# Kernel tuning notes

Measured on AMD Instinct MI355X. Metric: run time of the kernel, lower is better.

The kernel has to match this reference:

```python
import jax, jax.numpy as jnp
from jax import lax
import numpy as np

B, N, D_MODEL = 4, 2048, 768
D_INNER = 1536      # int(2.0 * d_model)
DT_RANK = 48        # ceil(768 / 16)
EPS = 1e-5


def setup_inputs() -> dict:
    key = jax.random.key(0)
    ks = jax.random.split(key, 9)
    x = jax.random.normal(ks[0], (B, N, D_MODEL), jnp.float32)
    # BFS order: a permutation of node ids
    sorted_index = jax.random.permutation(ks[1], N).astype(jnp.int32)
    # parent BFS position of node at BFS position i, must be < i; root (i=0) has -1
    pos = jnp.arange(N)
    r = jax.random.randint(ks[2], (N,), 0, N)
    sorted_parent = jnp.where(pos == 0, -1, r % jnp.maximum(pos, 1)).astype(jnp.int32)
    s = 0.02
    in_proj_w = jax.random.normal(ks[3], (D_MODEL, 2 * D_INNER), jnp.float32) * s
    x_proj_w = jax.random.normal(ks[4], (D_INNER, DT_RANK + 2), jnp.float32) * s
    dt_proj_w = jax.random.normal(ks[5], (DT_RANK, D_INNER), jnp.float32) * (DT_RANK ** -0.5)
    # dt bias init: softplus^{-1}(dt) with dt ~ LogUniform(1e-3, 1e-1)
    dt = jnp.exp(jax.random.uniform(ks[6], (D_INNER,)) * (np.log(0.1) - np.log(0.001)) + np.log(0.001))
    dt_proj_b = (dt + jnp.log(-jnp.expm1(-dt))).astype(jnp.float32)
    A_log = jnp.zeros((D_INNER,), jnp.float32)   # log(A=1) per original init (d_state=1)
    D_param = jnp.ones((D_INNER,), jnp.float32)
    ln_gamma = jnp.ones((D_INNER,), jnp.float32)
    ln_beta = jnp.zeros((D_INNER,), jnp.float32)
    out_proj_w = jax.random.normal(ks[7], (D_INNER, D_MODEL), jnp.float32) * s
    return dict(x=x, sorted_index=sorted_index, sorted_parent=sorted_parent,
                in_proj_w=in_proj_w, x_proj_w=x_proj_w, dt_proj_w=dt_proj_w,
                dt_proj_b=dt_proj_b, A_log=A_log, D_param=D_param,
                ln_gamma=ln_gamma, ln_beta=ln_beta, out_proj_w=out_proj_w)


def _tree_ssm_recurrence(dBx, dA, sorted_index, sorted_parent):
    """h[bfs i] = dA[node(i)] * h[parent_bfs(i)] + dBx[node(i)]. Inputs (B,N,Di) node-major."""
    b, n, di = dBx.shape
    dA_bfs = jnp.take(dA, sorted_index, axis=1)    # (B,N,Di) in BFS order
    dBx_bfs = jnp.take(dBx, sorted_index, axis=1)

    def step(h_buf, inp):
        t, par, dA_t, dBx_t = inp                   # dA_t/dBx_t: (B,Di)
        h_par = h_buf[:, jnp.maximum(par, 0)]       # (B,Di) gather at parent BFS pos
        h_par = jnp.where(par < 0, jnp.zeros_like(h_par), h_par)
        h_t = dA_t * h_par + dBx_t
        return h_buf.at[:, t].set(h_t), h_t

    xs = (jnp.arange(n), sorted_parent,
          dA_bfs.transpose(1, 0, 2), dBx_bfs.transpose(1, 0, 2))
    _, h_bfs = lax.scan(step, jnp.zeros((b, n, di), dBx.dtype), xs)
    # scatter BFS-order states back to node-id order
    h = jnp.zeros((b, n, di), dBx.dtype).at[:, sorted_index].set(h_bfs.transpose(1, 0, 2))
    return h


def reference(x, sorted_index, sorted_parent, in_proj_w, x_proj_w, dt_proj_w,
              dt_proj_b, A_log, D_param, ln_gamma, ln_beta, out_proj_w):
    xz = x @ in_proj_w                              # (B,N,2*Di)
    x_inner, z = jnp.split(xz, 2, axis=-1)
    z = jax.nn.silu(z)
    x_dbl = x_inner @ x_proj_w                      # (B,N,dt_rank+2)
    dt_lr, B_ssm, C_ssm = (x_dbl[..., :DT_RANK], x_dbl[..., DT_RANK:DT_RANK + 1],
                           x_dbl[..., DT_RANK + 1:DT_RANK + 2])
    dt = jax.nn.softplus(dt_lr @ dt_proj_w + dt_proj_b)  # (B,N,Di)
    As = -jnp.exp(A_log)                            # (Di,) negative
    dA = jnp.exp(dt * As)                           # (B,N,Di) in (0,1)
    dBx = dt * B_ssm * x_inner                      # (B,N,Di)
    h = _tree_ssm_recurrence(dBx, dA, sorted_index, sorted_parent)
    y = h * C_ssm + D_param * x_inner               # (B,N,Di)
    mu = jnp.mean(y, axis=-1, keepdims=True)
    var = jnp.mean(jnp.square(y - mu), axis=-1, keepdims=True)
    y = (y - mu) * lax.rsqrt(var + EPS) * ln_gamma + ln_beta
    y = y * z
    return y @ out_proj_w                           # (B,N,D)
```

## Files before the change

### kernel.cpp

```cpp
#include <hip/hip_runtime.h>
#include <math.h>


#define ROWS 8192
#define DIN 1536
#define DMOD 768
#define NSEQ 2048
#define DTR 48
#define NSPLIT 8

typedef __bf16 bfrag __attribute__((ext_vector_type(8)));
typedef float f4 __attribute__((ext_vector_type(4)));

__device__ __forceinline__ unsigned short f2bf(float f) {
  unsigned int u = __float_as_uint(f);
  unsigned int r = (u + 0x7fffu + ((u >> 16) & 1u)) >> 16;
  return (unsigned short)r;
}
__device__ __forceinline__ float bf2f(unsigned short h) {
  return __uint_as_float(((unsigned int)h) << 16);
}

__device__ __forceinline__ void gld_lds16(const void* g, void* l) {
  __builtin_amdgcn_global_load_lds((const __attribute__((address_space(1))) void*)g,
                                   (__attribute__((address_space(3))) void*)l, 16, 0, 0);
}

template <int MODE>
__global__ __launch_bounds__(256) void mfma_gemm(
    const unsigned short* __restrict__ A, const unsigned short* __restrict__ Bt,
    void* __restrict__ C0v, void* __restrict__ C1v, int K, int ldc) {
  __shared__ unsigned short As[128 * 32];
  __shared__ unsigned short Bs[128 * 32];
  const int tid = threadIdx.x;
  const int w = tid >> 6, l = tid & 63;
  const int quad = l >> 4, l16 = l & 15;
  const int wrow = (w >> 1) * 64, wcol = (w & 1) * 64;
  const int row0 = blockIdx.y * 128, col0 = blockIdx.x * 128;

  f4 acc[4][4];
#pragma unroll
  for (int i = 0; i < 4; i++)
#pragma unroll
    for (int j = 0; j < 4; j++) acc[i][j] = (f4){0.f, 0.f, 0.f, 0.f};

  const int arow = row0 + w * 16 + (l >> 2);
  const int brow = col0 + w * 16 + (l >> 2);
  const int kcol = (((l & 3) ^ ((l >> 2) & 3)) * 8);
  const int qs = (quad ^ (l16 & 3)) * 8;

  for (int k0 = 0; k0 < K; k0 += 32) {
#pragma unroll
    for (int r = 0; r < 2; r++) {
      gld_lds16(A + (size_t)(arow + r * 64) * K + k0 + kcol,
                (char*)As + r * 4096 + w * 1024);
      gld_lds16(Bt + (size_t)(brow + r * 64) * K + k0 + kcol,
                (char*)Bs + r * 4096 + w * 1024);
    }
    __syncthreads();
    bfrag af[4], bf[4];
#pragma unroll
    for (int i = 0; i < 4; i++)
      af[i] = *(const bfrag*)(const void*)(As + (wrow + i * 16 + l16) * 32 + qs);
#pragma unroll
    for (int j = 0; j < 4; j++)
      bf[j] = *(const bfrag*)(const void*)(Bs + (wcol + j * 16 + l16) * 32 + qs);
#pragma unroll
    for (int i = 0; i < 4; i++)
#pragma unroll
      for (int j = 0; j < 4; j++)
        acc[i][j] = __builtin_amdgcn_mfma_f32_16x16x32_bf16(af[i], bf[j], acc[i][j], 0, 0, 0);
    __syncthreads();
  }

  if (MODE == 0) {
    float* C0 = (float*)C0v;
    const int ccol = col0 + wcol + l16;
#pragma unroll
    for (int i = 0; i < 4; i++) {
      const int rb = row0 + wrow + i * 16 + quad * 4;
#pragma unroll
      for (int j = 0; j < 4; j++)
#pragma unroll
        for (int r = 0; r < 4; r++)
          C0[(size_t)(rb + r) * ldc + ccol + j * 16] = acc[i][j][r];
    }
  } else {
    const bool is_z = (col0 >= DIN);
    unsigned short* dst = is_z ? (unsigned short*)C1v : (unsigned short*)C0v;
    const int cbase = col0 + wcol + l16 - (is_z ? DIN : 0);
#pragma unroll
    for (int i = 0; i < 4; i++) {
      const int rb = row0 + wrow + i * 16 + quad * 4;
#pragma unroll
      for (int j = 0; j < 4; j++)
#pragma unroll
        for (int r = 0; r < 4; r++) {
          float v = acc[i][j][r];
          if (is_z) v = v / (1.f + __expf(-v));
          dst[(size_t)(rb + r) * DIN + cbase + j * 16] = f2bf(v);
        }
    }
  }
}

__global__ __launch_bounds__(1024) void prep1_kernel(
    const int* __restrict__ sidx, const int* __restrict__ spar,
    int* __restrict__ SLOT_PACK, int* __restrict__ SLOTINV,
    int* __restrict__ LSTART, int* __restrict__ NLEV,
    const float* __restrict__ x, unsigned short* __restrict__ Xbf,
    const float* __restrict__ xpw, unsigned short* __restrict__ XPW,
    const float* __restrict__ dtw, unsigned short* __restrict__ DTWb,
    const float* __restrict__ A_log, float* __restrict__ negA) {
  const int bi = blockIdx.x;
  const int tid = threadIdx.x;
  if (bi == 0) {
    __shared__ int par[2048], idx[2048], ancA[2048], ancB[2048], rnkA[2048], rnkB[2048];
    __shared__ int dmax;
    for (int i = tid; i < 2048; i += 1024) {
      const int p = spar[i];
      par[i] = p;
      idx[i] = sidx[i];
      ancA[i] = (p < 0) ? -1 : p;
      rnkA[i] = (p < 0) ? 0 : 1;
    }
    if (tid == 0) dmax = 0;
    __syncthreads();
    for (int r = 0; r < 11; r++) {
      int* ca = (r & 1) ? ancB : ancA;
      int* cr = (r & 1) ? rnkB : rnkA;
      int* na = (r & 1) ? ancA : ancB;
      int* nr = (r & 1) ? rnkA : rnkB;
      for (int i = tid; i < 2048; i += 1024) {
        const int a = ca[i], rv = cr[i];
        if (a >= 0) {
          nr[i] = rv + cr[a];
          na[i] = ca[a];
        } else {
          nr[i] = rv;
          na[i] = a;
        }
      }
      __syncthreads();
    }
    for (int i = tid; i < 2048; i += 1024) ancA[i] = 0;
    __syncthreads();
    for (int i = tid; i < 2048; i += 1024) {
      atomicAdd(&ancA[rnkB[i]], 1);
      atomicMax(&dmax, rnkB[i]);
    }
    __syncthreads();
    for (int s = 0; s < 11; s++) {
      const int off = 1 << s;
      int* cur = (s & 1) ? ancB : ancA;
      int* nxt = (s & 1) ? ancA : ancB;
      for (int i = tid; i < 2048; i += 1024) {
        int v = cur[i];
        if (i >= off) v += cur[i - off];
        nxt[i] = v;
      }
      __syncthreads();
    }
    for (int i = tid; i < 2049; i += 1024) {
      const int v = (i == 0) ? 0 : ancB[i - 1];
      LSTART[i] = v;
      if (i < 2048) rnkA[i] = v;
    }
    if (tid == 0) NLEV[0] = dmax + 1;
    __syncthreads();
    for (int i = tid; i < 2048; i += 1024) {
      const int d = rnkB[i];
      const int slot = atomicAdd(&rnkA[d], 1);
      const int node = idx[i];
      const int p = par[i];
      const int pn = (p < 0) ? -1 : idx[p];
      SLOT_PACK[slot] = node | ((pn + 1) << 12);
      SLOTINV[node] = slot;
    }
  } else if (bi < 1 + 1536) {
    const int i = ((bi - 1) * 1024 + tid) * 4;
    const float4 v = *(const float4*)(x + i);
    union { unsigned short h[4]; uint2 u; } pk;
    pk.h[0] = f2bf(v.x);
    pk.h[1] = f2bf(v.y);
    pk.h[2] = f2bf(v.z);
    pk.h[3] = f2bf(v.w);
    *(uint2*)(Xbf + i) = pk.u;
  } else if (bi < 1 + 1536 + 96) {
    const int i = (bi - 1537) * 1024 + tid;
    const int c = i / 1536, k = i % 1536;
    XPW[i] = (c < 50) ? f2bf(xpw[(size_t)k * 50 + c]) : (unsigned short)0;
  } else if (bi < 1 + 1536 + 96 + 96) {
    const int i = (bi - 1633) * 1024 + tid;
    const int d = i >> 6, k = i & 63;
    DTWb[i] = (k < 48) ? f2bf(dtw[(size_t)k * DIN + d]) : (unsigned short)0;
  } else {
    const int i = (bi - 1729) * 1024 + tid;
    if (i < DIN) negA[i] = -__expf(A_log[i]);
  }
}

__global__ __launch_bounds__(256) void prep2_kernel(
    const float* __restrict__ W1, unsigned short* __restrict__ W1t,
    const float* __restrict__ W2, unsigned short* __restrict__ W2t) {
  __shared__ float t[32][33];
  int idx = blockIdx.x;
  const float* W;
  unsigned short* Wt;
  int K, N, n0, k0;
  if (idx < 2304) {
    W = W1; Wt = W1t; K = DMOD; N = 2 * DIN;
    n0 = (idx % 96) * 32; k0 = (idx / 96) * 32;
  } else {
    idx -= 2304;
    W = W2; Wt = W2t; K = DIN; N = DMOD;
    n0 = (idx % 24) * 32; k0 = (idx / 24) * 32;
  }
  const int tx = threadIdx.x & 31, ty = threadIdx.x >> 5;
  for (int i = ty; i < 32; i += 8) t[i][tx] = W[(size_t)(k0 + i) * N + n0 + tx];
  __syncthreads();
  for (int i = ty; i < 32; i += 8)
    Wt[(size_t)(n0 + i) * K + k0 + tx] = f2bf(t[tx][i]);
}

__global__ __launch_bounds__(256) void xdbl_mfma(
    const unsigned short* __restrict__ XI, const unsigned short* __restrict__ XPW,
    float* __restrict__ XP) {
  __shared__ unsigned short As[128 * 32];
  __shared__ unsigned short Bs[64 * 32];
  const int tid = threadIdx.x;
  const int w = tid >> 6, l = tid & 63;
  const int quad = l >> 4, l16 = l & 15;
  const int split = blockIdx.x;
  const int row0 = blockIdx.y * 128;
  const int kbase = split * (DIN / NSPLIT);

  f4 acc[2][4];
#pragma unroll
  for (int i = 0; i < 2; i++)
#pragma unroll
    for (int j = 0; j < 4; j++) acc[i][j] = (f4){0.f, 0.f, 0.f, 0.f};

  const int srow = w * 16 + (l >> 2);
  const int kcol = (((l & 3) ^ ((l >> 2) & 3)) * 8);
  const int qs = (quad ^ (l16 & 3)) * 8;

  for (int c = 0; c < 6; c++) {
    const int k0 = kbase + c * 32;
#pragma unroll
    for (int r = 0; r < 2; r++) {
      gld_lds16(XI + (size_t)(row0 + srow + r * 64) * DIN + k0 + kcol,
                (char*)As + r * 4096 + w * 1024);
    }
    gld_lds16(XPW + (size_t)srow * DIN + k0 + kcol, (char*)Bs + w * 1024);
    __syncthreads();
    bfrag af[2], bf[4];
#pragma unroll
    for (int i = 0; i < 2; i++)
      af[i] = *(const bfrag*)(const void*)(As + (w * 32 + i * 16 + l16) * 32 + qs);
#pragma unroll
    for (int j = 0; j < 4; j++)
      bf[j] = *(const bfrag*)(const void*)(Bs + (j * 16 + l16) * 32 + qs);
#pragma unroll
    for (int i = 0; i < 2; i++)
#pragma unroll
      for (int j = 0; j < 4; j++)
        acc[i][j] = __builtin_amdgcn_mfma_f32_16x16x32_bf16(af[i], bf[j], acc[i][j], 0, 0, 0);
    __syncthreads();
  }

  float* dst = XP + (size_t)split * ROWS * 64 + (size_t)row0 * 64;
#pragma unroll
  for (int i = 0; i < 2; i++) {
    const int rb = w * 32 + i * 16 + quad * 4;
#pragma unroll
    for (int j = 0; j < 4; j++) {
      const int col = j * 16 + l16;
#pragma unroll
      for (int r = 0; r < 4; r++) dst[(size_t)(rb + r) * 64 + col] = acc[i][j][r];
    }
  }
}

__global__ __launch_bounds__(256) void xp_reduce(
    const float* __restrict__ XP, unsigned short* __restrict__ DTLRb,
    float* __restrict__ BCv, float* __restrict__ CCv) {
  const int i = blockIdx.x * 256 + threadIdx.x;
  const int row = i >> 4, c4 = (i & 15) * 4;
  const float* p = XP + (size_t)row * 64 + c4;
  float4 s = make_float4(0.f, 0.f, 0.f, 0.f);
#pragma unroll
  for (int sp = 0; sp < NSPLIT; sp++) {
    const float4 v = *(const float4*)(p + (size_t)sp * ROWS * 64);
    s.x += v.x;
    s.y += v.y;
    s.z += v.z;
    s.w += v.w;
  }
  if (c4 == 48) {
    BCv[row] = s.x;
    CCv[row] = s.y;
  }
  union { unsigned short h[4]; uint2 u; } pk;
  pk.h[0] = f2bf(s.x);
  pk.h[1] = f2bf(s.y);
  pk.h[2] = f2bf(s.z);
  pk.h[3] = f2bf(s.w);
  *(uint2*)(DTLRb + (size_t)row * 64 + c4) = pk.u;
}

__global__ __launch_bounds__(256) void dt_gemm(
    const unsigned short* __restrict__ DTLRb, const unsigned short* __restrict__ DTWb,
    const float* __restrict__ bias, const float* __restrict__ negA,
    const float* __restrict__ BCv, const unsigned short* __restrict__ XI,
    const int* __restrict__ SLOTINV,
    unsigned short* __restrict__ DAp, unsigned short* __restrict__ DBXp) {
  __shared__ unsigned short As[2][64 * 32];
  __shared__ unsigned short Bs[2][128 * 32];
  __shared__ int sinv[64];
  __shared__ float bcs[64];
  const int tid = threadIdx.x;
  const int w = tid >> 6, l = tid & 63;
  const int quad = l >> 4, l16 = l & 15;
  const int wrow = (w >> 1) * 32, wcol = (w & 1) * 64;
  const int row0 = blockIdx.y * 64, col0 = blockIdx.x * 128;
  const int p0 = row0 & (NSEQ - 1);
  const int bbase = row0 & ~(NSEQ - 1);
  const int srow = w * 16 + (l >> 2);
  const int koff = (((l & 3) ^ ((l >> 2) & 3)) * 8);
  const int qs = (quad ^ (l16 & 3)) * 8;

#pragma unroll
  for (int c = 0; c < 2; c++) {
    gld_lds16(DTLRb + (size_t)(row0 + srow) * 64 + c * 32 + koff,
              (char*)As[c] + w * 1024);
#pragma unroll
    for (int r = 0; r < 2; r++)
      gld_lds16(DTWb + (size_t)(col0 + srow + r * 64) * 64 + c * 32 + koff,
                (char*)Bs[c] + r * 4096 + w * 1024);
  }
  if (tid < 64) {
    sinv[tid] = SLOTINV[p0 + tid];
    bcs[tid] = BCv[row0 + tid];
  }
  __syncthreads();

  f4 acc[2][4];
#pragma unroll
  for (int i = 0; i < 2; i++)
#pragma unroll
    for (int j = 0; j < 4; j++) acc[i][j] = (f4){0.f, 0.f, 0.f, 0.f};

#pragma unroll
  for (int c = 0; c < 2; c++) {
    bfrag af[2], bf[4];
#pragma unroll
    for (int i = 0; i < 2; i++)
      af[i] = *(const bfrag*)(const void*)(As[c] + (wrow + i * 16 + l16) * 32 + qs);
#pragma unroll
    for (int j = 0; j < 4; j++)
      bf[j] = *(const bfrag*)(const void*)(Bs[c] + (wcol + j * 16 + l16) * 32 + qs);
#pragma unroll
    for (int i = 0; i < 2; i++)
#pragma unroll
      for (int j = 0; j < 4; j++)
        acc[i][j] = __builtin_amdgcn_mfma_f32_16x16x32_bf16(af[i], bf[j], acc[i][j], 0, 0, 0);
  }

  float bj[4], aj[4];
#pragma unroll
  for (int j = 0; j < 4; j++) {
    const int d = col0 + wcol + j * 16 + l16;
    bj[j] = bias[d];
    aj[j] = negA[d];
  }
#pragma unroll
  for (int i = 0; i < 2; i++) {
#pragma unroll
    for (int r = 0; r < 4; r++) {
      const int row_l = wrow + i * 16 + quad * 4 + r;
      const int row = row0 + row_l;
      const float bc = bcs[row_l];
      const size_t rp = (size_t)(bbase + sinv[row_l]) * DIN;
#pragma unroll
      for (int j = 0; j < 4; j++) {
        const int d = col0 + wcol + j * 16 + l16;
        const float s = acc[i][j][r] + bj[j];
        const float sp = fmaxf(s, 0.f) + __logf(1.f + __expf(-fabsf(s)));
        const float xi = bf2f(XI[(size_t)row * DIN + d]);
        DAp[rp + d] = f2bf(__expf(sp * aj[j]));
        DBXp[rp + d] = f2bf(sp * bc * xi);
      }
    }
  }
}

__global__ __launch_bounds__(256) void recur_kernel(
    const unsigned short* __restrict__ DAp, const unsigned short* __restrict__ DBXp,
    unsigned short* __restrict__ Hb,
    const int* __restrict__ SLOT_PACK, const int* __restrict__ LSTART,
    const int* __restrict__ NLEV) {
  __shared__ unsigned short hl[NSEQ * 16];
  __shared__ int spack[NSEQ];
  __shared__ int lst[258];
  const int tid = threadIdx.x;
  const int c8a = blockIdx.x * 2;
  const int b = c8a / 192;
  const int d8a = c8a % 192;
  const int nlev = NLEV[0];
  for (int i = tid; i < NSEQ; i += 256) spack[i] = SLOT_PACK[i];
  const int nl = (nlev + 1 < 258) ? nlev + 1 : 258;
  for (int i = tid; i < nl; i += 256) lst[i] = LSTART[i];
  __syncthreads();

  for (int L = 0; L < nlev; L++) {
    const int s0 = (L < 257) ? lst[L] : LSTART[L];
    const int s1 = (L + 1 < 258) ? lst[L + 1] : LSTART[L + 1];
    const int items = (s1 - s0) * 2;
    for (int it = tid; it < items; it += 256) {
      const int s = s0 + (it >> 1);
      const int ch = it & 1;
      const size_t goff = (size_t)(b * NSEQ + s) * DIN + (d8a + ch) * 8;
      union { uint4 u; unsigned short h[8]; } da, dbx, hpu, hvu;
      da.u = *(const uint4*)(DAp + goff);
      dbx.u = *(const uint4*)(DBXp + goff);
      const int pk = spack[s];
      const int node = pk & 4095;
      const int pn = (pk >> 12) - 1;
      float hp[8];
      if (pn >= 0) {
        hpu.u = *(const uint4*)(hl + pn * 16 + ch * 8);
#pragma unroll
        for (int e = 0; e < 8; e++) hp[e] = bf2f(hpu.h[e]);
      } else {
#pragma unroll
        for (int e = 0; e < 8; e++) hp[e] = 0.f;
      }
#pragma unroll
      for (int e = 0; e < 8; e++) {
        const float hv = fmaf(bf2f(da.h[e]), hp[e], bf2f(dbx.h[e]));
        hvu.h[e] = f2bf(hv);
      }
      *(uint4*)(hl + node * 16 + ch * 8) = hvu.u;
    }
    __syncthreads();
  }

  for (int i = tid; i < NSEQ * 2; i += 256) {
    const int node = i >> 1, ch = i & 1;
    *(uint4*)(Hb + (size_t)(b * NSEQ + node) * DIN + (d8a + ch) * 8) =
        *(const uint4*)(hl + node * 16 + ch * 8);
  }
}

__global__ __launch_bounds__(256) void ln_kernel(
    const unsigned short* __restrict__ Hb, const float* __restrict__ CCv,
    const unsigned short* __restrict__ XI, const float* __restrict__ Dp,
    const float* __restrict__ gamma, const float* __restrict__ beta,
    const unsigned short* __restrict__ Z, unsigned short* __restrict__ YLN) {
  const int row = blockIdx.x;
  const int tid = threadIdx.x;
  const float C = CCv[row];
  const unsigned short* hrow = Hb + (size_t)row * DIN;
  const unsigned short* xrow = XI + (size_t)row * DIN;
  float y[6];
  float s = 0.f, s2 = 0.f;
#pragma unroll
  for (int i = 0; i < 6; i++) {
    const int d = tid + i * 256;
    const float v = fmaf(bf2f(hrow[d]), C, Dp[d] * bf2f(xrow[d]));
    y[i] = v;
    s += v;
    s2 = fmaf(v, v, s2);
  }
#pragma unroll
  for (int off = 32; off >= 1; off >>= 1) {
    s += __shfl_down(s, off);
    s2 += __shfl_down(s2, off);
  }
  __shared__ float rs[4], rs2[4];
  const int w = tid >> 6;
  if ((tid & 63) == 0) {
    rs[w] = s;
    rs2[w] = s2;
  }
  __syncthreads();
  const float ts = rs[0] + rs[1] + rs[2] + rs[3];
  const float ts2 = rs2[0] + rs2[1] + rs2[2] + rs2[3];
  const float mu = ts * (1.f / 1536.f);
  const float var = ts2 * (1.f / 1536.f) - mu * mu;
  const float inv = rsqrtf(var + 1e-5f);
  unsigned short* yrow = YLN + (size_t)row * DIN;
  const unsigned short* zrow = Z + (size_t)row * DIN;
#pragma unroll
  for (int i = 0; i < 6; i++) {
    const int d = tid + i * 256;
    const float o = (y[i] - mu) * inv * gamma[d] + beta[d];
    yrow[d] = f2bf(o * bf2f(zrow[d]));
  }
}

extern "C" void kernel_launch(void* const* d_in, const int* in_sizes, int n_in,
                              void* d_out, int out_size, void* d_ws, size_t ws_size,
                              hipStream_t stream) {
  const float* x = (const float*)d_in[0];
  const int* sidx = (const int*)d_in[1];
  const int* spar = (const int*)d_in[2];
  const float* in_proj = (const float*)d_in[3];
  const float* x_proj = (const float*)d_in[4];
  const float* dt_proj = (const float*)d_in[5];
  const float* dt_b = (const float*)d_in[6];
  const float* A_log = (const float*)d_in[7];
  const float* Dp = (const float*)d_in[8];
  const float* gamma = (const float*)d_in[9];
  const float* beta = (const float*)d_in[10];
  const float* out_proj = (const float*)d_in[11];
  float* out = (float*)d_out;

  char* p = (char*)d_ws;
  const size_t RC = (size_t)ROWS * DIN;
  unsigned short* XI = (unsigned short*)p;   p += RC * 2;
  unsigned short* Z = (unsigned short*)p;    p += RC * 2;
  unsigned short* DAp = (unsigned short*)p;  p += RC * 2;
  unsigned short* DBXp = (unsigned short*)p; p += RC * 2;
  unsigned short* Hb = (unsigned short*)p;   p += RC * 2;
  float* XP = (float*)p;                     p += (size_t)NSPLIT * ROWS * 64 * 4;
  unsigned short* DTLRb = (unsigned short*)p; p += (size_t)ROWS * 64 * 2;
  float* BCv = (float*)p;                    p += ROWS * 4;
  float* CCv = (float*)p;                    p += ROWS * 4;
  float* negA = (float*)p;                   p += DIN * 4;
  unsigned short* Xbf = (unsigned short*)p;  p += (size_t)ROWS * DMOD * 2;
  unsigned short* W1t = (unsigned short*)p;  p += (size_t)2 * DIN * DMOD * 2;
  unsigned short* W2t = (unsigned short*)p;  p += (size_t)DMOD * DIN * 2;
  unsigned short* XPW = (unsigned short*)p;  p += (size_t)64 * DIN * 2;
  unsigned short* DTWb = (unsigned short*)p; p += (size_t)DIN * 64 * 2;
  int* ipart = (int*)p;
  int* SLOT_PACK = ipart;
  int* SLOTINV = ipart + 2048;
  int* LSTART = ipart + 4096;
  int* NLEV = ipart + 4096 + 2049;
  unsigned short* YLN = DAp;

  prep1_kernel<<<1731, 1024, 0, stream>>>(sidx, spar, SLOT_PACK, SLOTINV,
                                          LSTART, NLEV, x, Xbf, x_proj, XPW,
                                          dt_proj, DTWb, A_log, negA);
  prep2_kernel<<<3456, 256, 0, stream>>>(in_proj, W1t, out_proj, W2t);
  mfma_gemm<1><<<dim3(24, 64), 256, 0, stream>>>(Xbf, W1t, XI, Z, DMOD, DIN);
  xdbl_mfma<<<dim3(NSPLIT, 64), 256, 0, stream>>>(XI, XPW, XP);
  xp_reduce<<<ROWS * 16 / 256, 256, 0, stream>>>(XP, DTLRb, BCv, CCv);
  dt_gemm<<<dim3(12, 128), 256, 0, stream>>>(DTLRb, DTWb, dt_b, negA, BCv, XI,
                                             SLOTINV, DAp, DBXp);
  recur_kernel<<<384, 256, 0, stream>>>(DAp, DBXp, Hb, SLOT_PACK, LSTART, NLEV);
  ln_kernel<<<ROWS, 256, 0, stream>>>(Hb, CCv, XI, Dp, gamma, beta, Z, YLN);
  mfma_gemm<0><<<dim3(6, 64), 256, 0, stream>>>(YLN, W2t, out, nullptr, DIN, DMOD);
}
```

Before: 326.6 us.

## Replace in_proj GEMM with 256x256-tile, double-buffered, phase-interleaved MFMA kernel

Swaps the 128x128 in_proj GEMM for a 512-thread kernel using 256x256 output tiles and K=64 steps. It double-buffers LDS with direct global-to-LDS loads and a swizzled layout, and interleaves the load stages with four MFMA phases using barriers and setprio. The aim is more data reuse per tile and better overlap of memory traffic with MFMA work. The cost is a large LDS footprint (128 KB) that limits occupancy, plus fewer blocks that can leave a tail wave.

```diff
diff --git a/kernel.cpp b/kernel.cpp
--- a/kernel.cpp
+++ b/kernel.cpp
@@ -24,6 +24,167 @@
 __device__ __forceinline__ void gld_lds16(const void* g, void* l) {
   __builtin_amdgcn_global_load_lds((const __attribute__((address_space(1))) void*)g,
                                    (__attribute__((address_space(3))) void*)l, 16, 0, 0);
+}
+
+__device__ __forceinline__ void barx() {
+  asm volatile("" ::: "memory");
+  __builtin_amdgcn_sched_barrier(0);
+  __builtin_amdgcn_s_barrier();
+  __builtin_amdgcn_sched_barrier(0);
+  asm volatile("" ::: "memory");
+}
+
+__global__ __launch_bounds__(512, 2) void gemm256_silu(
+    const unsigned short* __restrict__ A, const unsigned short* __restrict__ Bt,
+    unsigned short* __restrict__ XI, unsigned short* __restrict__ Z, int K) {
+  __shared__ unsigned short lds[2][2][256 * 64];
+  const int tid = threadIdx.x;
+  const int w = tid >> 6, l = tid & 63;
+  const int quad = l >> 4, l16 = l & 15;
+  const int wr = w >> 2, wc = w & 3;
+  const int row0 = blockIdx.y * 256, col0 = blockIdx.x * 256;
+  const int nt = K >> 6;
+
+  const int srow = tid >> 3;
+  const int schunk = ((tid & 7) ^ (srow & 7)) * 8;
+  const unsigned short* aS = A + (size_t)(row0 + srow) * K + schunk;
+  const unsigned short* bS = Bt + (size_t)(col0 + srow) * K + schunk;
+
+#define STG(bufi, isb, q, kt)                                               \
+  gld_lds16(((isb) ? bS : aS) + (size_t)((q) * 64) * K + (size_t)(kt) * 64, \
+            (char*)&lds[bufi][isb][(q) * 4096] + w * 1024)
+
+  const int arow = (wr * 128 + l16) * 64;
+  const int brow = (wc * 64 + l16) * 64;
+  int cs[2];
+  cs[0] = (quad ^ (l16 & 7)) * 8;
+  cs[1] = ((4 + quad) ^ (l16 & 7)) * 8;
+
+#define RDA(m, ks) (*(const bfrag*)(const void*)(LA + arow + (m) * 1024 + cs[ks]))
+#define RDB(n, ks) (*(const bfrag*)(const void*)(LB + brow + (n) * 1024 + cs[ks]))
+
+  f4 acc[8][4];
+#pragma unroll
+  for (int m = 0; m < 8; m++)
+#pragma unroll
+    for (int n = 0; n < 4; n++) acc[m][n] = (f4){0.f, 0.f, 0.f, 0.f};
+
+  const int kt1 = (nt > 1) ? 1 : 0;
+#pragma unroll
+  for (int q = 0; q < 4; q++) STG(0, 0, q, 0);
+#pragma unroll
+  for (int q = 0; q < 4; q++) STG(0, 1, q, 0);
+#pragma unroll
+  for (int q = 0; q < 4; q++) STG(1, 0, q, kt1);
+  asm volatile("s_waitcnt vmcnt(4)" ::: "memory");
+  barx();
+
+  for (int t = 0; t < nt; ++t) {
+    const int b = t & 1;
+    const unsigned short* LA = &lds[b][0][0];
+    const unsigned short* LB = &lds[b][1][0];
+    const int kB = (t + 1 < nt) ? (t + 1) : (nt - 1);
+    const int kA = (t + 2 < nt) ? (t + 2) : (nt - 1);
+    bfrag af[4][2], bfr[4][2];
+
+#pragma unroll
+    for (int m = 0; m < 4; m++) {
+      af[m][0] = RDA(m, 0);
+      af[m][1] = RDA(m, 1);
+    }
+#pragma unroll
+    for (int n = 0; n < 2; n++) {
+      bfr[n][0] = RDB(n, 0);
+      bfr[n][1] = RDB(n, 1);
+    }
+    STG(b ^ 1, 1, 0, kB);
+    STG(b ^ 1, 1, 1, kB);
+    barx();
+    __builtin_amdgcn_s_setprio(1);
+#pragma unroll
+    for (int m = 0; m < 4; m++)
+#pragma unroll
+      for (int n = 0; n < 2; n++) {
+        acc[m][n] = __builtin_amdgcn_mfma_f32_16x16x32_bf16(af[m][0], bfr[n][0], acc[m][n], 0, 0, 0);
+        acc[m][n] = __builtin_amdgcn_mfma_f32_16x16x32_bf16(af[m][1], bfr[n][1], acc[m][n], 0, 0, 0);
+      }
+    __builtin_amdgcn_s_setprio(0);
+    barx();
+
+#pragma unroll
+    for (int n = 2; n < 4; n++) {
+      bfr[n][0] = RDB(n, 0);
+      bfr[n][1] = RDB(n, 1);
+    }
+    STG(b ^ 1, 1, 2, kB);
+    STG(b ^ 1, 1, 3, kB);
+    barx();
+    __builtin_amdgcn_s_setprio(1);
+#pragma unroll
+    for (int m = 0; m < 4; m++)
+#pragma unroll
+      for (int n = 2; n < 4; n++) {
+        acc[m][n] = __builtin_amdgcn_mfma_f32_16x16x32_bf16(af[m][0], bfr[n][0], acc[m][n], 0, 0, 0);
+        acc[m][n] = __builtin_amdgcn_mfma_f32_16x16x32_bf16(af[m][1], bfr[n][1], acc[m][n], 0, 0, 0);
+      }
+    __builtin_amdgcn_s_setprio(0);
+    barx();
+
+#pragma unroll
+    for (int m = 0; m < 4; m++) {
+      af[m][0] = RDA(m + 4, 0);
+      af[m][1] = RDA(m + 4, 1);
+    }
+    STG(b, 0, 0, kA);
+    STG(b, 0, 2, kA);
+    barx();
+    __builtin_amdgcn_s_setprio(1);
+#pragma unroll
+    for (int m = 0; m < 4; m++)
+#pragma unroll
+      for (int n = 0; n < 2; n++) {
+        acc[m + 4][n] = __builtin_amdgcn_mfma_f32_16x16x32_bf16(af[m][0], bfr[n][0], acc[m + 4][n], 0, 0, 0);
+        acc[m + 4][n] = __builtin_amdgcn_mfma_f32_16x16x32_bf16(af[m][1], bfr[n][1], acc[m + 4][n], 0, 0, 0);
+      }
+    __builtin_amdgcn_s_setprio(0);
+    barx();
+
+    STG(b, 0, 1, kA);
+    STG(b, 0, 3, kA);
+    barx();
+    __builtin_amdgcn_s_setprio(1);
+#pragma unroll
+    for (int m = 0; m < 4; m++)
+#pragma unroll
+      for (int n = 2; n < 4; n++) {
+        acc[m + 4][n] = __builtin_amdgcn_mfma_f32_16x16x32_bf16(af[m][0], bfr[n][0], acc[m + 4][n], 0, 0, 0);
+        acc[m + 4][n] = __builtin_amdgcn_mfma_f32_16x16x32_bf16(af[m][1], bfr[n][1], acc[m + 4][n], 0, 0, 0);
+      }
+    __builtin_amdgcn_s_setprio(0);
+    asm volatile("s_waitcnt vmcnt(4)" ::: "memory");
+    barx();
+  }
+  asm volatile("s_waitcnt vmcnt(0)" ::: "memory");
+
+#undef STG
+#undef RDA
+#undef RDB
+
+  const bool is_z = (col0 >= DIN);
+  unsigned short* dst = is_z ? Z : XI;
+  const int cb = col0 + wc * 64 + l16 - (is_z ? DIN : 0);
+#pragma unroll
+  for (int m = 0; m < 8; m++) {
+    const int rb = row0 + wr * 128 + m * 16 + quad * 4;
+#pragma unroll
+    for (int n = 0; n < 4; n++)
+#pragma unroll
+      for (int r = 0; r < 4; r++) {
+        float v = acc[m][n][r];
+        if (is_z) v = v / (1.f + __expf(-v));
+        dst[(size_t)(rb + r) * DIN + cb + n * 16] = f2bf(v);
+      }
+  }
 }
 
 template <int MODE>
@@ -545,7 +706,7 @@
                                           LSTART, NLEV, x, Xbf, x_proj, XPW,
                                           dt_proj, DTWb, A_log, negA);
   prep2_kernel<<<3456, 256, 0, stream>>>(in_proj, W1t, out_proj, W2t);
-  mfma_gemm<1><<<dim3(24, 64), 256, 0, stream>>>(Xbf, W1t, XI, Z, DMOD, DIN);
+  gemm256_silu<<<dim3(12, 32), 512, 0, stream>>>(Xbf, W1t, XI, Z, DMOD);
   xdbl_mfma<<<dim3(NSPLIT, 64), 256, 0, stream>>>(XI, XPW, XP);
   xp_reduce<<<ROWS * 16 / 256, 256, 0, stream>>>(XP, DTLRb, BCv, CCv);
   dt_gemm<<<dim3(12, 128), 256, 0, stream>>>(DTLRb, DTWb, dt_b, negA, BCv, XI,
```

After: 325.8 us. About the same (-0.2%).
